# Optimization experiments

Hardware: AMD Instinct MI355X
Metric: run time of the kernel (lower is better)

The kernel has to match this reference:

```python
import jax, jax.numpy as jnp
import numpy as np

N, D, H, L, B, DFF = 100000, 256, 8, 64, 4096, 1024
HD = D // H  # head_dim
EPS = 1e-5


def _xavier(k, shape):
    lim = (6.0 / (shape[0] + shape[1])) ** 0.5
    return jax.random.uniform(k, shape, jnp.float32, -lim, lim)


def setup_inputs() -> dict:
    key = jax.random.key(0)
    ks = jax.random.split(key, 12)
    batch = jax.random.randint(ks[0], (B,), 0, N)
    nei_idx = jax.random.randint(ks[1], (B, L), 0, N)
    # faithful to neis_ = [[k] + neighbor[k] ...]: self node is first neighbor
    nei_idx = nei_idx.at[:, 0].set(batch)
    lengths = jax.random.randint(ks[2], (B,), 1, L + 1)
    nei_mask = jnp.arange(L)[None, :] >= lengths[:, None]  # True = NaN padding
    embeddings = jax.random.normal(ks[3], (N, D), jnp.float32)
    return {
        "batch": batch, "nei_idx": nei_idx, "nei_mask": nei_mask,
        "embeddings": embeddings,
        "Wq": _xavier(ks[4], (D, D)), "bq": jnp.zeros((D,), jnp.float32),
        "Wk": _xavier(ks[5], (D, D)), "bk": jnp.zeros((D,), jnp.float32),
        "Wv": _xavier(ks[6], (D, D)), "bv": jnp.zeros((D,), jnp.float32),
        "Wo": _xavier(ks[7], (D, D)), "bo": jnp.zeros((D,), jnp.float32),
        "W1": _xavier(ks[8], (D, DFF)), "b1": jnp.zeros((DFF,), jnp.float32),
        "W2": _xavier(ks[9], (DFF, D)), "b2": jnp.zeros((D,), jnp.float32),
        "ln1_w": jnp.ones((D,), jnp.float32), "ln1_b": jnp.zeros((D,), jnp.float32),
        "ln2_w": jnp.ones((D,), jnp.float32), "ln2_b": jnp.zeros((D,), jnp.float32),
    }


def _layer_norm(y, w, b):
    mu = y.mean(-1, keepdims=True)
    var = ((y - mu) ** 2).mean(-1, keepdims=True)
    return (y - mu) / jnp.sqrt(var + EPS) * w + b


def reference(batch, nei_idx, nei_mask, embeddings,
              Wq, bq, Wk, bk, Wv, bv, Wo, bo,
              W1, b1, W2, b2, ln1_w, ln1_b, ln2_w, ln2_b):
    x = embeddings[batch]        # [B, D]  query-node embeddings
    nei = embeddings[nei_idx]    # [B, L, D] gathered (padded) neighbor embeds
    q = ((x @ Wq + bq) * (HD ** -0.5)).reshape(B, H, HD)
    k = (nei @ Wk + bk).reshape(B, L, H, HD)
    v = (nei @ Wv + bv).reshape(B, L, H, HD)
    scores = jnp.einsum('bhd,blhd->bhl', q, k)          # single-query attn
    scores = jnp.where(nei_mask[:, None, :], -jnp.inf, scores)
    att = jax.nn.softmax(scores, axis=-1)               # [B, H, L]
    attout = jnp.einsum('bhl,blhd->bhd', att, v).reshape(B, D) @ Wo + bo
    s = _layer_norm(x + attout, ln1_w, ln1_b)
    # note: original applies relu after BOTH linear1 and linear2
    f = jax.nn.relu(jax.nn.relu(s @ W1 + b1) @ W2 + b2)
    return _layer_norm(s + f, ln2_w, ln2_b)
```

## Files before the change

### kernel.cpp

```cpp
#include <hip/hip_runtime.h>
#include <hip/hip_bf16.h>
#include <math.h>

#define BQ   4096
#define D    256
#define NH   8
#define HD   32
#define LN_  64
#define DFF  1024
#define EPSV 1e-5f
#define QSCALE 0.17677669529663687f

typedef __attribute__((ext_vector_type(8))) short short8;
typedef __attribute__((ext_vector_type(4))) float f32x4;

#define ESWZ(row, byte) ((byte) ^ (((row) & 7) << 4))

__device__ __forceinline__ float wave_sum(float v){
#pragma unroll
  for (int off = 32; off; off >>= 1) v += __shfl_xor(v, off, 64);
  return v;
}
__device__ __forceinline__ unsigned short f2bf(float f){
  unsigned int u = __float_as_uint(f);
  unsigned int r = (u + 0x7FFFu + ((u >> 16) & 1u)) >> 16;
  return (unsigned short)r;
}

__global__ __launch_bounds__(256) void k_prep(
    const float* __restrict__ Wq, const float* __restrict__ Wk,
    const float* __restrict__ Wv, const float* __restrict__ Wo,
    const float* __restrict__ W1, const float* __restrict__ W2,
    const float* __restrict__ bq, const float* __restrict__ bv,
    const float* __restrict__ bo,
    const int* __restrict__ batch, const float* __restrict__ emb,
    const unsigned int* __restrict__ maskw,
    unsigned short* __restrict__ W1t, unsigned short* __restrict__ W2t,
    unsigned short* __restrict__ Mt, unsigned short* __restrict__ Gt,
    float* __restrict__ pb, float* __restrict__ bo2,
    float* __restrict__ X, unsigned short* __restrict__ Xb,
    int* __restrict__ flags){
  __shared__ float smem[4224];
  const int bid = blockIdx.x;
  const int tid = threadIdx.x;

  if (bid < 128){
    const float* src; unsigned short* dst; int K, N, t0;
    if (bid < 64){ src = W1; dst = W1t; K = 256;  N = 1024; t0 = bid; }
    else         { src = W2; dst = W2t; K = 1024; N = 256;  t0 = bid - 64; }
    const int ntx = N / 64;
    const int k0 = (t0 / ntx) * 64, n0 = (t0 % ntx) * 64;
    float (*Ts)[65] = (float(*)[65])smem;
    {
      int r = tid >> 2, c4 = (tid & 3) * 16;
#pragma unroll
      for (int i = 0; i < 4; i++)
        *(float4*)&Ts[r][c4 + i * 4] = *(const float4*)(src + (size_t)(k0 + r) * N + n0 + c4 + i * 4);
    }
    __syncthreads();
    {
      int n = tid >> 2, kc = (tid & 3) * 16;
      unsigned int pk[8];
#pragma unroll
      for (int i = 0; i < 8; i++){
        unsigned int lo = f2bf(Ts[kc + 2 * i][n]);
        unsigned int hi = f2bf(Ts[kc + 2 * i + 1][n]);
        pk[i] = lo | (hi << 16);
      }
      unsigned short* orow = dst + (size_t)(n0 + n) * K + k0 + kc;
      *(uint4*)(orow)     = *(uint4*)&pk[0];
      *(uint4*)(orow + 8) = *(uint4*)&pk[4];
    }
    return;
  }
  if (bid < 256){
    int t0 = bid - 128;
    int hd0 = (t0 & 31) * 64, c0 = (t0 >> 5) * 64;
    int h = hd0 >> 8, d0 = hd0 & 255;
    float (*WqS)[33] = (float(*)[33])smem;
    float (*WkS)[33] = (float(*)[33])(smem + 64 * 33);
#pragma unroll
    for (int s = 0; s < 2; s++){
      int idx = tid + s * 256;
      int row = idx >> 3, c4 = (idx & 7) * 4;
      *(float4*)&WqS[row][c4] = *(const float4*)(Wq + (size_t)(c0 + row) * 256 + h * 32 + c4);
      *(float4*)&WkS[row][c4] = *(const float4*)(Wk + (size_t)(d0 + row) * 256 + h * 32 + c4);
    }
    __syncthreads();
    int jo = (tid >> 4) * 4, io = (tid & 15) * 4;
    float acc[4][4];
#pragma unroll
    for (int j = 0; j < 4; j++)
#pragma unroll
      for (int i = 0; i < 4; i++) acc[j][i] = 0.f;
#pragma unroll
    for (int t = 0; t < 32; t++){
#pragma unroll
      for (int j = 0; j < 4; j++){
        float kv = WkS[jo + j][t];
#pragma unroll
        for (int i = 0; i < 4; i++) acc[j][i] = fmaf(kv, WqS[io + i][t], acc[j][i]);
      }
    }
#pragma unroll
    for (int j = 0; j < 4; j++){
      uint2 o;
      o.x = (unsigned)f2bf(acc[j][0] * QSCALE) | ((unsigned)f2bf(acc[j][1] * QSCALE) << 16);
      o.y = (unsigned)f2bf(acc[j][2] * QSCALE) | ((unsigned)f2bf(acc[j][3] * QSCALE) << 16);
      *(uint2*)(Mt + (size_t)(hd0 + jo + j) * 256 + c0 + io) = o;
    }
    if (c0 == 0 && tid < 64){
      float s = 0.f;
#pragma unroll
      for (int t = 0; t < 32; t++) s = fmaf(WkS[tid][t], bq[h * 32 + t], s);
      pb[hd0 + tid] = s * QSCALE;
    }
    return;
  }
  if (bid < 384){
    int t0 = bid - 256;
    int hd0 = (t0 & 31) * 64, n0 = (t0 >> 5) * 64;
    int h = hd0 >> 8, d0 = hd0 & 255;
    float (*WvS)[33] = (float(*)[33])smem;
    float (*WoS)[65] = (float(*)[65])(smem + 64 * 33);
#pragma unroll
    for (int s = 0; s < 2; s++){
      int idx = tid + s * 256;
      int row = idx >> 3, c4 = (idx & 7) * 4;
      *(float4*)&WvS[row][c4] = *(const float4*)(Wv + (size_t)(d0 + row) * 256 + h * 32 + c4);
      int row2 = idx >> 4, c42 = (idx & 15) * 4;
      *(float4*)&WoS[row2][c42] = *(const float4*)(Wo + (size_t)(h * 32 + row2) * 256 + n0 + c42);
    }
    __syncthreads();
    int jo = (tid >> 4) * 4, io = (tid & 15) * 4;
    float acc[4][4];
#pragma unroll
    for (int i = 0; i < 4; i++)
#pragma unroll
      for (int j = 0; j < 4; j++) acc[i][j] = 0.f;
#pragma unroll
    for (int t = 0; t < 32; t++){
#pragma unroll
      for (int i = 0; i < 4; i++){
        float ov = WoS[t][io + i];
#pragma unroll
        for (int j = 0; j < 4; j++) acc[i][j] = fmaf(ov, WvS[jo + j][t], acc[i][j]);
      }
    }
#pragma unroll
    for (int i = 0; i < 4; i++){
      uint2 o;
      o.x = (unsigned)f2bf(acc[i][0]) | ((unsigned)f2bf(acc[i][1]) << 16);
      o.y = (unsigned)f2bf(acc[i][2]) | ((unsigned)f2bf(acc[i][3]) << 16);
      *(uint2*)(Gt + (size_t)(n0 + io + i) * 2048 + hd0 + jo) = o;
    }
    return;
  }
  if (bid == 384){
    int n = tid;
    float s = bo[n];
    for (int j = 0; j < 256; j++) s = fmaf(bv[j], Wo[(size_t)j * 256 + n], s);
    bo2[n] = s;
    return;
  }
  if (bid < 641){
    int idx = (bid - 385) * 256 + tid;
    unsigned int v = maskw[idx];
    int bits = 0;
    if (v == 0x3F800000u) bits = 2;
    else if (v & 0xFFFFFF00u) bits = 1;
    int b2 = __any(bits & 2) ? 2 : 0;
    int b1 = __any(bits & 1) ? 1 : 0;
    if ((tid & 63) == 0 && (b1 | b2)) atomicOr(flags, b1 | b2);
    return;
  }
  {
    int gid = (bid - 641) * 256 + tid;
    int b = gid >> 6, c = gid & 63;
    float4 v = ((const float4*)(emb + (size_t)batch[b] * D))[c];
    ((float4*)(X + (size_t)b * D))[c] = v;
    uint2 p;
    p.x = (unsigned)f2bf(v.x) | ((unsigned)f2bf(v.y) << 16);
    p.y = (unsigned)f2bf(v.z) | ((unsigned)f2bf(v.w) << 16);
    ((uint2*)Xb)[gid] = p;
  }
}

template<int BM, int BN, int EPI, bool OUTBF>
__global__ __launch_bounds__(256) void k_mgemm(const unsigned short* __restrict__ A,
                                               const unsigned short* __restrict__ Bt,
                                               const float* __restrict__ bias,
                                               void* __restrict__ Cout,
                                               int M, int N, int K){
  constexpr int BK = 64;
  constexpr int WM = BM / 2, WN = BN / 2;
  constexpr int MR = WM / 16, NR = WN / 16;
  __shared__ __align__(16) unsigned short As[BM * BK];
  __shared__ __align__(16) unsigned short Bs[BN * BK];
  char* ab = (char*)As; char* bb = (char*)Bs;
  const int tid = threadIdx.x;
  const int w = tid >> 6, lane = tid & 63;
  const int wm = w >> 1, wn = w & 1;
  const int row0 = blockIdx.y * BM, col0 = blockIdx.x * BN;
  f32x4 acc[MR][NR];
#pragma unroll
  for (int m = 0; m < MR; m++)
#pragma unroll
    for (int n = 0; n < NR; n++) acc[m][n] = (f32x4){0.f, 0.f, 0.f, 0.f};

  constexpr int AIT = BM * 8 / 256;
  constexpr int BIT = BN * 8 / 256;

  for (int k0 = 0; k0 < K; k0 += BK){
#pragma unroll
    for (int s = 0; s < AIT; s++){
      int c = s * 256 + tid;
      int r = c >> 3, jj = c & 7;
      uint4 v = *(const uint4*)(A + (size_t)(row0 + r) * K + k0 + jj * 8);
      *(uint4*)(ab + ESWZ(r, r * 128 + jj * 16)) = v;
    }
#pragma unroll
    for (int s = 0; s < BIT; s++){
      int c = s * 256 + tid;
      int r = c >> 3, jj = c & 7;
      uint4 v = *(const uint4*)(Bt + (size_t)(col0 + r) * K + k0 + jj * 8);
      *(uint4*)(bb + ESWZ(r, r * 128 + jj * 16)) = v;
    }
    __syncthreads();
#pragma unroll
    for (int kk = 0; kk < 2; kk++){
      short8 af[MR], bf[NR];
#pragma unroll
      for (int m = 0; m < MR; m++){
        int r = wm * WM + m * 16 + (lane & 15);
        af[m] = *(const short8*)(ab + ESWZ(r, r * 128 + (kk * 4 + (lane >> 4)) * 16));
      }
#pragma unroll
      for (int n = 0; n < NR; n++){
        int r = wn * WN + n * 16 + (lane & 15);
        bf[n] = *(const short8*)(bb + ESWZ(r, r * 128 + (kk * 4 + (lane >> 4)) * 16));
      }
#pragma unroll
      for (int m = 0; m < MR; m++)
#pragma unroll
        for (int n = 0; n < NR; n++)
          acc[m][n] = __builtin_amdgcn_mfma_f32_16x16x32_bf16(af[m], bf[n], acc[m][n], 0, 0, 0);
    }
    __syncthreads();
  }
#pragma unroll
  for (int m = 0; m < MR; m++){
#pragma unroll
    for (int n = 0; n < NR; n++){
      int col = col0 + wn * WN + n * 16 + (lane & 15);
      float bsv = bias[col];
      int rbase = row0 + wm * WM + m * 16 + (lane >> 4) * 4;
#pragma unroll
      for (int r = 0; r < 4; r++){
        float v = acc[m][n][r] + bsv;
        if (EPI == 3) v = fmaxf(v, 0.f);
        if (OUTBF) ((unsigned short*)Cout)[(size_t)(rbase + r) * N + col] = f2bf(v);
        else       ((float*)Cout)[(size_t)(rbase + r) * N + col] = v;
      }
    }
  }
}

__global__ __launch_bounds__(256) void k_attn(const int* __restrict__ nei_idx,
                                              const void* __restrict__ nei_mask,
                                              const int* __restrict__ flagp,
                                              const float* __restrict__ emb,
                                              const unsigned short* __restrict__ Pb,
                                              unsigned short* __restrict__ Cb){
  const int b = blockIdx.x;
  const int tid = threadIdx.x;
  const int w = tid >> 6, lane = tid & 63;
  __shared__ __align__(16) unsigned short Ebf[64 * 256];
  __shared__ __align__(16) unsigned short Pl[9 * 256];
  __shared__ float sc[NH * LN_];
  __shared__ int   nid[LN_];
  __shared__ float mskv[LN_];
  char* eb = (char*)Ebf;
  char* pl = (char*)Pl;

  const int fl = flagp[0];
  const int mf = (fl & 2) ? 2 : ((fl & 1) ? 1 : 0);
  if (tid < LN_){
    nid[tid] = nei_idx[(size_t)b * LN_ + tid];
    bool m;
    if (mf == 1)      m = ((const unsigned char*)nei_mask)[(size_t)b * LN_ + tid] != 0;
    else if (mf == 2) m = ((const float*)nei_mask)[(size_t)b * LN_ + tid] != 0.f;
    else              m = ((const int*)nei_mask)[(size_t)b * LN_ + tid] != 0;
    mskv[tid] = m ? 1.f : 0.f;
  }
  {
    int r = tid >> 5, cb16 = (tid & 31) * 16;
    uint4 v = *(const uint4*)((const char*)Pb + (size_t)b * 4096 + r * 512 + cb16);
    *(uint4*)(pl + ESWZ(r, r * 512 + cb16)) = v;
    if (tid < 64) *(uint2*)(pl + 8 * 512 + tid * 8) = make_uint2(0u, 0u);
  }
  __syncthreads();

#pragma unroll
  for (int half = 0; half < 2; half++){
    float4 vr[8];
#pragma unroll
    for (int i = 0; i < 8; i++){
      int l = w * 16 + half * 8 + i;
      vr[i] = ((const float4*)(emb + (size_t)nid[l] * D))[lane];
    }
#pragma unroll
    for (int i = 0; i < 8; i++){
      int l = w * 16 + half * 8 + i;
      uint2 p;
      p.x = (unsigned)f2bf(vr[i].x) | ((unsigned)f2bf(vr[i].y) << 16);
      p.y = (unsigned)f2bf(vr[i].z) | ((unsigned)f2bf(vr[i].w) << 16);
      *(uint2*)(eb + ESWZ(l, l * 512 + lane * 8)) = p;
    }
  }
  __syncthreads();

  {
    const int hr = lane & 15;
    const int arow = hr < 8 ? hr : 8;
    const int bl = w * 16 + (lane & 15);
    const int koff = (lane >> 4) * 16;
    f32x4 acc = {0.f, 0.f, 0.f, 0.f};
#pragma unroll
    for (int kk = 0; kk < 8; kk++){
      short8 af = *(const short8*)(pl + ESWZ(arow, arow * 512 + kk * 64 + koff));
      short8 bf = *(const short8*)(eb + ESWZ(bl, bl * 512 + kk * 64 + koff));
      acc = __builtin_amdgcn_mfma_f32_16x16x32_bf16(af, bf, acc, 0, 0, 0);
    }
    int l = w * 16 + (lane & 15);
    int hb = (lane >> 4) * 4;
    if (hb < 8){
#pragma unroll
      for (int r = 0; r < 4; r++) sc[(hb + r) * LN_ + l] = acc[r];
    }
  }
  __syncthreads();

  {
    int h = tid >> 5, j = tid & 31;
    float v0 = mskv[j]      > 0.5f ? -INFINITY : sc[h * LN_ + j];
    float v1 = mskv[j + 32] > 0.5f ? -INFINITY : sc[h * LN_ + j + 32];
    float m = fmaxf(v0, v1);
#pragma unroll
    for (int off = 16; off; off >>= 1) m = fmaxf(m, __shfl_xor(m, off, 64));
    float e0 = __expf(v0 - m), e1 = __expf(v1 - m);
    float s = e0 + e1;
#pragma unroll
    for (int off = 16; off; off >>= 1) s += __shfl_xor(s, off, 64);
    float inv = 1.f / s;
    sc[h * LN_ + j]      = e0 * inv;
    sc[h * LN_ + j + 32] = e1 * inv;
  }
  __syncthreads();

  {
    const int h0 = w * 2, h1 = w * 2 + 1;
    float4 a0 = make_float4(0.f, 0.f, 0.f, 0.f);
    float4 a1 = make_float4(0.f, 0.f, 0.f, 0.f);
#pragma unroll 8
    for (int l = 0; l < 64; l++){
      uint2 raw = *(const uint2*)(eb + ESWZ(l, l * 512 + lane * 8));
      float e0 = __uint_as_float(raw.x << 16);
      float e1 = __uint_as_float(raw.x & 0xFFFF0000u);
      float e2 = __uint_as_float(raw.y << 16);
      float e3 = __uint_as_float(raw.y & 0xFFFF0000u);
      float t0 = sc[h0 * LN_ + l], t1 = sc[h1 * LN_ + l];
      a0.x = fmaf(t0, e0, a0.x); a0.y = fmaf(t0, e1, a0.y);
      a0.z = fmaf(t0, e2, a0.z); a0.w = fmaf(t0, e3, a0.w);
      a1.x = fmaf(t1, e0, a1.x); a1.y = fmaf(t1, e1, a1.y);
      a1.z = fmaf(t1, e2, a1.z); a1.w = fmaf(t1, e3, a1.w);
    }
    uint2 o0, o1;
    o0.x = (unsigned)f2bf(a0.x) | ((unsigned)f2bf(a0.y) << 16);
    o0.y = (unsigned)f2bf(a0.z) | ((unsigned)f2bf(a0.w) << 16);
    o1.x = (unsigned)f2bf(a1.x) | ((unsigned)f2bf(a1.y) << 16);
    o1.y = (unsigned)f2bf(a1.z) | ((unsigned)f2bf(a1.w) << 16);
    *(uint2*)((char*)Cb + (size_t)b * 4096 + h0 * 512 + lane * 8) = o0;
    *(uint2*)((char*)Cb + (size_t)b * 4096 + h1 * 512 + lane * 8) = o1;
  }
}

__global__ __launch_bounds__(256) void k_ln(const float* __restrict__ A,
                                            const float* __restrict__ Bv,
                                            const float* __restrict__ w,
                                            const float* __restrict__ bi,
                                            float* __restrict__ out,
                                            unsigned short* __restrict__ outb){
  const int row = blockIdx.x, tid = threadIdx.x;
  const int wv = tid >> 6, lane = tid & 63;
  __shared__ float red[8];
  float v = A[(size_t)row * D + tid] + Bv[(size_t)row * D + tid];
  float s = wave_sum(v);
  if (lane == 0) red[wv] = s;
  __syncthreads();
  float mu = (red[0] + red[1] + red[2] + red[3]) * (1.f / D);
  float d = v - mu;
  float s2 = wave_sum(d * d);
  if (lane == 0) red[4 + wv] = s2;
  __syncthreads();
  float var = (red[4] + red[5] + red[6] + red[7]) * (1.f / D);
  float res = d * rsqrtf(var + EPSV) * w[tid] + bi[tid];
  out[(size_t)row * D + tid] = res;
  if (outb) outb[(size_t)row * D + tid] = f2bf(res);
}

extern "C" void kernel_launch(void* const* d_in, const int* in_sizes, int n_in,
                              void* d_out, int out_size, void* d_ws, size_t ws_size,
                              hipStream_t stream){
  (void)in_sizes; (void)n_in; (void)out_size; (void)ws_size;
  const int*   batch    = (const int*)d_in[0];
  const int*   nei_idx  = (const int*)d_in[1];
  const void*  nei_mask = d_in[2];
  const float* emb      = (const float*)d_in[3];
  const float* Wq = (const float*)d_in[4];  const float* bq = (const float*)d_in[5];
  const float* Wk = (const float*)d_in[6];
  const float* Wv = (const float*)d_in[8];  const float* bv = (const float*)d_in[9];
  const float* Wo = (const float*)d_in[10]; const float* bo = (const float*)d_in[11];
  const float* W1 = (const float*)d_in[12]; const float* b1 = (const float*)d_in[13];
  const float* W2 = (const float*)d_in[14]; const float* b2 = (const float*)d_in[15];
  const float* ln1w = (const float*)d_in[16]; const float* ln1b = (const float*)d_in[17];
  const float* ln2w = (const float*)d_in[18]; const float* ln2b = (const float*)d_in[19];

  float* ws = (float*)d_ws;
  float* X  = ws;
  float* Y  = ws + (size_t)1 * 1048576;
  float* S  = ws + (size_t)2 * 1048576;
  float* F  = ws + (size_t)3 * 1048576;
  unsigned short* Pbf = (unsigned short*)(ws + (size_t)4 * 1048576);
  unsigned short* Cb  = Pbf;
  unsigned short* Sb  = (unsigned short*)(ws + (size_t)8 * 1048576);
  unsigned short* HHb = (unsigned short*)(ws + (size_t)9 * 1048576);
  unsigned short* Xb  = (unsigned short*)(ws + (size_t)11 * 1048576);
  char* wb = (char*)(ws + (size_t)12 * 1048576);
  unsigned short* W1t = (unsigned short*)(wb);
  unsigned short* W2t = (unsigned short*)(wb + (512u << 10));
  unsigned short* Mt  = (unsigned short*)(wb + (1024u << 10));
  unsigned short* Gt  = (unsigned short*)(wb + (2048u << 10));
  float* pbv  = (float*)(wb + (3072u << 10));
  float* bo2  = (float*)(wb + (3072u << 10) + 8192);
  int*   flags = (int*)(wb + (3072u << 10) + 16384);
  float* out = (float*)d_out;

  hipMemsetAsync(flags, 0, 4, stream);
  k_prep<<<1665, 256, 0, stream>>>(Wq, Wk, Wv, Wo, W1, W2, bq, bv, bo,
                                   batch, emb, (const unsigned int*)nei_mask,
                                   W1t, W2t, Mt, Gt, pbv, bo2, X, Xb, flags);
  k_mgemm<128, 64, 2, true><<<dim3(2048 / 64, BQ / 128), 256, 0, stream>>>(Xb, Mt, pbv, Pbf, BQ, 2048, 256);
  k_attn<<<BQ, 256, 0, stream>>>(nei_idx, nei_mask, flags, emb, Pbf, Cb);
  k_mgemm<64, 64, 2, false><<<dim3(D / 64, BQ / 64), 256, 0, stream>>>(Cb, Gt, bo2, Y, BQ, D, 2048);
  k_ln<<<BQ, 256, 0, stream>>>(X, Y, ln1w, ln1b, S, Sb);
  k_mgemm<128, 64, 3, true><<<dim3(DFF / 64, BQ / 128), 256, 0, stream>>>(Sb, W1t, b1, HHb, BQ, DFF, 256);
  k_mgemm<64, 64, 3, false><<<dim3(D / 64, BQ / 64), 256, 0, stream>>>(HHb, W2t, b2, F, BQ, D, DFF);
  k_ln<<<BQ, 256, 0, stream>>>(S, F, ln2w, ln2b, out, nullptr);
}
```

Before: 132.4 us.

## Prefetch GEMM tiles into registers, hoist attention gathers, drop flag memset

The GEMM kernel now loads the next K tile from global memory into registers while the current tile is computed from shared memory, hiding global load latency behind MFMA work. The attention kernel issues all 16 neighbor-row gathers per wave up front, overlapping them with the mask-format reduction and the projection-row load instead of waiting on a shared index array. The mask-type flag is now written as one value per block into an array that attention reduces, which removes the memset launch and the global atomics. Costs are more registers per thread in both kernels, which may lower occupancy.

```diff
diff --git a/kernel.cpp b/kernel.cpp
--- a/kernel.cpp
+++ b/kernel.cpp
@@ -39,7 +39,7 @@
     unsigned short* __restrict__ Mt, unsigned short* __restrict__ Gt,
     float* __restrict__ pb, float* __restrict__ bo2,
     float* __restrict__ X, unsigned short* __restrict__ Xb,
-    int* __restrict__ flags){
+    int* __restrict__ flagsArr){
   __shared__ float smem[4224];
   const int bid = blockIdx.x;
   const int tid = threadIdx.x;
@@ -164,6 +164,9 @@
     return;
   }
   if (bid < 641){
+    int* df = (int*)smem;
+    if (tid == 0) df[0] = 0;
+    __syncthreads();
     int idx = (bid - 385) * 256 + tid;
     unsigned int v = maskw[idx];
     int bits = 0;
@@ -171,7 +174,9 @@
     else if (v & 0xFFFFFF00u) bits = 1;
     int b2 = __any(bits & 2) ? 2 : 0;
     int b1 = __any(bits & 1) ? 1 : 0;
-    if ((tid & 63) == 0 && (b1 | b2)) atomicOr(flags, b1 | b2);
+    if ((tid & 63) == 0 && (b1 | b2)) atomicOr(df, b1 | b2);
+    __syncthreads();
+    if (tid == 0) flagsArr[bid - 385] = df[0];
     return;
   }
   {
@@ -185,6 +190,35 @@
     ((uint2*)Xb)[gid] = p;
   }
 }
+
+#define MG_LOADA(s, k0) { int c = (s) * 256 + tid; int r = c >> 3, jj = c & 7; \
+  avr[s] = *(const uint4*)(A + (size_t)(row0 + r) * K + (k0) + jj * 8); }
+#define MG_LOADB(s, k0) { int c = (s) * 256 + tid; int r = c >> 3, jj = c & 7; \
+  bvr[s] = *(const uint4*)(Bt + (size_t)(col0 + r) * K + (k0) + jj * 8); }
+#define MG_STOREA(s) { int c = (s) * 256 + tid; int r = c >> 3, jj = c & 7; \
+  *(uint4*)(ab + ESWZ(r, r * 128 + jj * 16)) = avr[s]; }
+#define MG_STOREB(s) { int c = (s) * 256 + tid; int r = c >> 3, jj = c & 7; \
+  *(uint4*)(bb + ESWZ(r, r * 128 + jj * 16)) = bvr[s]; }
+#define MG_COMPUTE() \
+  _Pragma("unroll") \
+  for (int kk = 0; kk < 2; kk++){ \
+    short8 af[MR], bf[NR]; \
+    _Pragma("unroll") \
+    for (int m = 0; m < MR; m++){ \
+      int r = wm * WM + m * 16 + (lane & 15); \
+      af[m] = *(const short8*)(ab + ESWZ(r, r * 128 + (kk * 4 + (lane >> 4)) * 16)); \
+    } \
+    _Pragma("unroll") \
+    for (int n = 0; n < NR; n++){ \
+      int r = wn * WN + n * 16 + (lane & 15); \
+      bf[n] = *(const short8*)(bb + ESWZ(r, r * 128 + (kk * 4 + (lane >> 4)) * 16)); \
+    } \
+    _Pragma("unroll") \
+    for (int m = 0; m < MR; m++) \
+      _Pragma("unroll") \
+      for (int n = 0; n < NR; n++) \
+        acc[m][n] = __builtin_amdgcn_mfma_f32_16x16x32_bf16(af[m], bf[n], acc[m][n], 0, 0, 0); \
+  }
 
 template<int BM, int BN, int EPI, bool OUTBF>
 __global__ __launch_bounds__(256) void k_mgemm(const unsigned short* __restrict__ A,
@@ -195,6 +229,8 @@
   constexpr int BK = 64;
   constexpr int WM = BM / 2, WN = BN / 2;
   constexpr int MR = WM / 16, NR = WN / 16;
+  constexpr int AIT = BM * 8 / 256;
+  constexpr int BIT = BN * 8 / 256;
   __shared__ __align__(16) unsigned short As[BM * BK];
   __shared__ __align__(16) unsigned short Bs[BN * BK];
   char* ab = (char*)As; char* bb = (char*)Bs;
@@ -208,46 +244,31 @@
 #pragma unroll
     for (int n = 0; n < NR; n++) acc[m][n] = (f32x4){0.f, 0.f, 0.f, 0.f};
 
-  constexpr int AIT = BM * 8 / 256;
-  constexpr int BIT = BN * 8 / 256;
-
-  for (int k0 = 0; k0 < K; k0 += BK){
-#pragma unroll
-    for (int s = 0; s < AIT; s++){
-      int c = s * 256 + tid;
-      int r = c >> 3, jj = c & 7;
-      uint4 v = *(const uint4*)(A + (size_t)(row0 + r) * K + k0 + jj * 8);
-      *(uint4*)(ab + ESWZ(r, r * 128 + jj * 16)) = v;
-    }
-#pragma unroll
-    for (int s = 0; s < BIT; s++){
-      int c = s * 256 + tid;
-      int r = c >> 3, jj = c & 7;
-      uint4 v = *(const uint4*)(Bt + (size_t)(col0 + r) * K + k0 + jj * 8);
-      *(uint4*)(bb + ESWZ(r, r * 128 + jj * 16)) = v;
-    }
-    __syncthreads();
-#pragma unroll
-    for (int kk = 0; kk < 2; kk++){
-      short8 af[MR], bf[NR];
-#pragma unroll
-      for (int m = 0; m < MR; m++){
-        int r = wm * WM + m * 16 + (lane & 15);
-        af[m] = *(const short8*)(ab + ESWZ(r, r * 128 + (kk * 4 + (lane >> 4)) * 16));
-      }
-#pragma unroll
-      for (int n = 0; n < NR; n++){
-        int r = wn * WN + n * 16 + (lane & 15);
-        bf[n] = *(const short8*)(bb + ESWZ(r, r * 128 + (kk * 4 + (lane >> 4)) * 16));
-      }
-#pragma unroll
-      for (int m = 0; m < MR; m++)
-#pragma unroll
-        for (int n = 0; n < NR; n++)
-          acc[m][n] = __builtin_amdgcn_mfma_f32_16x16x32_bf16(af[m], bf[n], acc[m][n], 0, 0, 0);
-    }
-    __syncthreads();
-  }
+  uint4 avr[AIT], bvr[BIT];
+#pragma unroll
+  for (int s = 0; s < AIT; s++) MG_LOADA(s, 0)
+#pragma unroll
+  for (int s = 0; s < BIT; s++) MG_LOADB(s, 0)
+#pragma unroll
+  for (int s = 0; s < AIT; s++) MG_STOREA(s)
+#pragma unroll
+  for (int s = 0; s < BIT; s++) MG_STOREB(s)
+  __syncthreads();
+  for (int k0 = BK; k0 < K; k0 += BK){
+#pragma unroll
+    for (int s = 0; s < AIT; s++) MG_LOADA(s, k0)
+#pragma unroll
+    for (int s = 0; s < BIT; s++) MG_LOADB(s, k0)
+    MG_COMPUTE()
+    __syncthreads();
+#pragma unroll
+    for (int s = 0; s < AIT; s++) MG_STOREA(s)
+#pragma unroll
+    for (int s = 0; s < BIT; s++) MG_STOREB(s)
+    __syncthreads();
+  }
+  MG_COMPUTE()
+
 #pragma unroll
   for (int m = 0; m < MR; m++){
 #pragma unroll
@@ -268,7 +289,7 @@
 
 __global__ __launch_bounds__(256) void k_attn(const int* __restrict__ nei_idx,
                                               const void* __restrict__ nei_mask,
-                                              const int* __restrict__ flagp,
+                                              const int* __restrict__ flagsArr,
                                               const float* __restrict__ emb,
                                               const unsigned short* __restrict__ Pb,
                                               unsigned short* __restrict__ Cb){
@@ -278,46 +299,48 @@
   __shared__ __align__(16) unsigned short Ebf[64 * 256];
   __shared__ __align__(16) unsigned short Pl[9 * 256];
   __shared__ float sc[NH * LN_];
-  __shared__ int   nid[LN_];
   __shared__ float mskv[LN_];
+  __shared__ int   fred[4];
   char* eb = (char*)Ebf;
   char* pl = (char*)Pl;
 
-  const int fl = flagp[0];
-  const int mf = (fl & 2) ? 2 : ((fl & 1) ? 1 : 0);
+  {
+    int f = flagsArr[tid];
+#pragma unroll
+    for (int off = 32; off; off >>= 1) f |= __shfl_xor(f, off, 64);
+    if (lane == 0) fred[w] = f;
+  }
+  float4 vr[16];
+#pragma unroll
+  for (int i = 0; i < 16; i++){
+    int nid = nei_idx[(size_t)b * LN_ + w * 16 + i];
+    vr[i] = ((const float4*)(emb + (size_t)nid * D))[lane];
+  }
+  {
+    int r = tid >> 5, cb16 = (tid & 31) * 16;
+    uint4 v = *(const uint4*)((const char*)Pb + (size_t)b * 4096 + r * 512 + cb16);
+    *(uint4*)(pl + ESWZ(r, r * 512 + cb16)) = v;
+  }
+  if (tid < 64) *(uint2*)(pl + 8 * 512 + tid * 8) = make_uint2(0u, 0u);
+  __syncthreads();
+
+#pragma unroll
+  for (int i = 0; i < 16; i++){
+    int l = w * 16 + i;
+    uint2 p;
+    p.x = (unsigned)f2bf(vr[i].x) | ((unsigned)f2bf(vr[i].y) << 16);
+    p.y = (unsigned)f2bf(vr[i].z) | ((unsigned)f2bf(vr[i].w) << 16);
+    *(uint2*)(eb + ESWZ(l, l * 512 + lane * 8)) = p;
+  }
   if (tid < LN_){
-    nid[tid] = nei_idx[(size_t)b * LN_ + tid];
+    int fl = fred[0] | fred[1] | fred[2] | fred[3];
+    int mf = (fl & 2) ? 2 : ((fl & 1) ? 1 : 0);
     bool m;
     if (mf == 1)      m = ((const unsigned char*)nei_mask)[(size_t)b * LN_ + tid] != 0;
     else if (mf == 2) m = ((const float*)nei_mask)[(size_t)b * LN_ + tid] != 0.f;
     else              m = ((const int*)nei_mask)[(size_t)b * LN_ + tid] != 0;
     mskv[tid] = m ? 1.f : 0.f;
   }
-  {
-    int r = tid >> 5, cb16 = (tid & 31) * 16;
-    uint4 v = *(const uint4*)((const char*)Pb + (size_t)b * 4096 + r * 512 + cb16);
-    *(uint4*)(pl + ESWZ(r, r * 512 + cb16)) = v;
-    if (tid < 64) *(uint2*)(pl + 8 * 512 + tid * 8) = make_uint2(0u, 0u);
-  }
-  __syncthreads();
-
-#pragma unroll
-  for (int half = 0; half < 2; half++){
-    float4 vr[8];
-#pragma unroll
-    for (int i = 0; i < 8; i++){
-      int l = w * 16 + half * 8 + i;
-      vr[i] = ((const float4*)(emb + (size_t)nid[l] * D))[lane];
-    }
-#pragma unroll
-    for (int i = 0; i < 8; i++){
-      int l = w * 16 + half * 8 + i;
-      uint2 p;
-      p.x = (unsigned)f2bf(vr[i].x) | ((unsigned)f2bf(vr[i].y) << 16);
-      p.y = (unsigned)f2bf(vr[i].z) | ((unsigned)f2bf(vr[i].w) << 16);
-      *(uint2*)(eb + ESWZ(l, l * 512 + lane * 8)) = p;
-    }
-  }
   __syncthreads();
 
   {
@@ -332,11 +355,10 @@
       short8 bf = *(const short8*)(eb + ESWZ(bl, bl * 512 + kk * 64 + koff));
       acc = __builtin_amdgcn_mfma_f32_16x16x32_bf16(af, bf, acc, 0, 0, 0);
     }
-    int l = w * 16 + (lane & 15);
     int hb = (lane >> 4) * 4;
     if (hb < 8){
 #pragma unroll
-      for (int r = 0; r < 4; r++) sc[(hb + r) * LN_ + l] = acc[r];
+      for (int r = 0; r < 4; r++) sc[(hb + r) * LN_ + bl] = acc[r];
     }
   }
   __syncthreads();
@@ -443,15 +465,14 @@
   unsigned short* Gt  = (unsigned short*)(wb + (2048u << 10));
   float* pbv  = (float*)(wb + (3072u << 10));
   float* bo2  = (float*)(wb + (3072u << 10) + 8192);
-  int*   flags = (int*)(wb + (3072u << 10) + 16384);
+  int*   flagsArr = (int*)(wb + (3072u << 10) + 16384);
   float* out = (float*)d_out;
 
-  hipMemsetAsync(flags, 0, 4, stream);
   k_prep<<<1665, 256, 0, stream>>>(Wq, Wk, Wv, Wo, W1, W2, bq, bv, bo,
                                    batch, emb, (const unsigned int*)nei_mask,
-                                   W1t, W2t, Mt, Gt, pbv, bo2, X, Xb, flags);
+                                   W1t, W2t, Mt, Gt, pbv, bo2, X, Xb, flagsArr);
   k_mgemm<128, 64, 2, true><<<dim3(2048 / 64, BQ / 128), 256, 0, stream>>>(Xb, Mt, pbv, Pbf, BQ, 2048, 256);
-  k_attn<<<BQ, 256, 0, stream>>>(nei_idx, nei_mask, flags, emb, Pbf, Cb);
+  k_attn<<<BQ, 256, 0, stream>>>(nei_idx, nei_mask, flagsArr, emb, Pbf, Cb);
   k_mgemm<64, 64, 2, false><<<dim3(D / 64, BQ / 64), 256, 0, stream>>>(Cb, Gt, bo2, Y, BQ, D, 2048);
   k_ln<<<BQ, 256, 0, stream>>>(X, Y, ln1w, ln1b, S, Sb);
   k_mgemm<128, 64, 3, true><<<dim3(DFF / 64, BQ / 128), 256, 0, stream>>>(Sb, W1t, b1, HHb, BQ, DFF, 256);
```

Measured after the change: 217.6 us. 64.3% more time.
